# Optimization experiments

Hardware: AMD Instinct MI355X
Metric: run time of the kernel (lower is better)

The kernel has to match this reference:

```python
import jax, jax.numpy as jnp
import numpy as np

B, P, K = 32, 1000, 40          # events, hits per event, kNN neighbors
N = B * P                        # total nodes
IN_C, D, S = 64, 32, 3           # in_channels, d_shape, space_dimensions
EPS = 1e-5


def _bn(x, g, b):
    # BatchNorm1d in training mode: batch statistics over the node axis
    m = x.mean(0)
    v = x.var(0)
    return (x - m) * jax.lax.rsqrt(v + EPS) * g + b


def setup_inputs() -> dict:
    key = jax.random.key(0)
    ks = jax.random.split(key, 16)

    def xavier(k, shape):
        lim = float(np.sqrt(6.0 / (shape[0] + shape[1])))
        return jax.random.uniform(k, shape, minval=-lim, maxval=lim, dtype=jnp.float32)

    return {
        "x": jax.random.normal(ks[0], (N, IN_C), dtype=jnp.float32),
        "original_coords": jax.random.normal(ks[1], (N, S), dtype=jnp.float32),
        "batch": jnp.repeat(jnp.arange(B, dtype=jnp.int64), P),
        # pre-gravnet MLP
        "pre_w1": xavier(ks[2], (IN_C, D)), "pre_b1": jnp.zeros((D,), jnp.float32),
        "pre_w2": xavier(ks[3], (D, D)),   "pre_b2": jnp.zeros((D,), jnp.float32),
        "bn1_g": jnp.ones((D,), jnp.float32), "bn1_b": jnp.zeros((D,), jnp.float32),
        # GravNetConv linears
        "lin_s_w": xavier(ks[4], (D, S)),  "lin_s_b": jnp.zeros((S,), jnp.float32),
        "lin_h_w": xavier(ks[5], (D, D)),  "lin_h_b": jnp.zeros((D,), jnp.float32),
        "out1_w": xavier(ks[6], (D, D)),                      # no bias (PyG lin_out1)
        "out2_w": xavier(ks[7], (2 * D, D)), "out2_b": jnp.zeros((D,), jnp.float32),
        # post-gravnet MLP (input = out_channels + space + d_shape = 67)
        "post_w1": xavier(ks[8], (D + S + D, D)), "post_b1": jnp.zeros((D,), jnp.float32),
        "post_w2": xavier(ks[9], (D, D)),         "post_b2": jnp.zeros((D,), jnp.float32),
        "bn2_g": jnp.ones((D,), jnp.float32), "bn2_b": jnp.zeros((D,), jnp.float32),
    }


def reference(x, original_coords, batch,
              pre_w1, pre_b1, pre_w2, pre_b2, bn1_g, bn1_b,
              lin_s_w, lin_s_b, lin_h_w, lin_h_b,
              out1_w, out2_w, out2_b,
              post_w1, post_b1, post_w2, post_b2, bn2_g, bn2_b):
    # pre-MLP + BN
    h = jax.nn.elu(jax.nn.elu(x @ pre_w1 + pre_b1) @ pre_w2 + pre_b2)
    h = _bn(h, bn1_g, bn1_b)
    x_input = h

    # GravNetConv: learned space + feature projections
    s = h @ lin_s_w + lin_s_b            # [N, S] gncoords
    feat = h @ lin_h_w + lin_h_b         # [N, D]

    sb = s.reshape(B, P, S)
    fb = feat.reshape(B, P, D)
    # dynamic kNN within each event (includes self, as in torch_cluster knn)
    d2 = jnp.sum((sb[:, :, None, :] - sb[:, None, :, :]) ** 2, axis=-1)  # [B,P,P]
    neg_d2, idx = jax.lax.top_k(-d2, K)                                   # [B,P,K]
    w = jnp.exp(10.0 * neg_d2)           # exp(-10 * d^2) edge weights

    neigh = jax.vmap(lambda f, i: f[i])(fb, idx)  # [B,P,K,D] gather
    msg = neigh * w[..., None]
    aggr = jnp.concatenate([msg.mean(axis=2), msg.max(axis=2)], axis=-1)  # [B,P,2D]
    aggr = aggr.reshape(N, 2 * D)

    xgn = h @ out1_w + aggr @ out2_w + out2_b   # [N, D]

    # concat + post-MLP + BN
    cat = jnp.concatenate([xgn, s, x_input], axis=1)  # [N, D+S+D]
    out = jax.nn.elu(jax.nn.elu(cat @ post_w1 + post_b1) @ post_w2 + post_b2)
    out = _bn(out, bn2_g, bn2_b)
    return out
```

## Files before the change

### kernel.cpp

```cpp
#include <hip/hip_runtime.h>
#include <math.h>

#define NN 32000
#define PP 1000
#define KK 40
#define INC 64
#define DD 32
#define EPSV 1e-5

#define OB_H64 0UL
#define OB_S64 8192000UL
#define OB_F32 8960000UL
#define OB_A32 13056000UL
#define OB_P1  21248000UL
#define OB_P2  21504000UL
#define OB_S32 21760000UL
#define OB_ST1 22144000UL
#define OB_ST2 22144512UL

__device__ __forceinline__ double elud(double v){ return v > 0.0 ? v : expm1(v); }
__device__ __forceinline__ float eluf(float v){ return v > 0.f ? v : expm1f(v); }

__global__ __launch_bounds__(128) void k_pre(const float* __restrict__ x,
    const float* __restrict__ w1, const float* __restrict__ b1,
    const float* __restrict__ w2, const float* __restrict__ b2,
    char* __restrict__ ws)
{
  __shared__ double lw1[INC*DD];
  __shared__ double lw2[DD*DD];
  __shared__ double lb1[DD], lb2[DD];
  __shared__ double wpart[2][64];
  int tid = threadIdx.x;
  int nodeBase = blockIdx.x * 64;
  for (int i = tid; i < INC*DD; i += 128) lw1[i] = (double)w1[i];
  for (int i = tid; i < DD*DD; i += 128) lw2[i] = (double)w2[i];
  if (tid < DD){ lb1[tid] = (double)b1[tid]; lb2[tid] = (double)b2[tid]; }
  __syncthreads();

  int nl = tid >> 1, half = tid & 1;
  int node = nodeBase + nl;
  const float* xr = x + (size_t)node * INC;
  double acc[16];
#pragma unroll
  for (int c = 0; c < 16; ++c) acc[c] = lb1[half*16 + c];
#pragma unroll 4
  for (int k = 0; k < INC; ++k){
    double xv = (double)xr[k];
#pragma unroll
    for (int c = 0; c < 16; ++c) acc[c] = fma(xv, lw1[k*DD + half*16 + c], acc[c]);
  }
  double h1o[16];
#pragma unroll
  for (int c = 0; c < 16; ++c) h1o[c] = elud(acc[c]);
  double h1f[DD];
#pragma unroll
  for (int i = 0; i < 16; ++i){
    double p = __shfl_xor(h1o[i], 1);
    h1f[i]      = half ? p : h1o[i];
    h1f[16 + i] = half ? h1o[i] : p;
  }
#pragma unroll
  for (int c = 0; c < 16; ++c) acc[c] = lb2[half*16 + c];
#pragma unroll 4
  for (int k = 0; k < DD; ++k){
    double hk = h1f[k];
#pragma unroll
    for (int c = 0; c < 16; ++c) acc[c] = fma(hk, lw2[k*DD + half*16 + c], acc[c]);
  }
  double h2[16];
#pragma unroll
  for (int c = 0; c < 16; ++c) h2[c] = elud(acc[c]);
  double* hT = (double*)(ws + OB_H64);
#pragma unroll
  for (int c = 0; c < 16; ++c) hT[(size_t)(half*16 + c)*NN + node] = h2[c];

  double s[16], q[16];
#pragma unroll
  for (int i = 0; i < 16; ++i){ s[i] = h2[i]; q[i] = h2[i]*h2[i]; }
#pragma unroll
  for (int o = 2; o <= 32; o <<= 1){
#pragma unroll
    for (int i = 0; i < 16; ++i){ s[i] += __shfl_xor(s[i], o); q[i] += __shfl_xor(q[i], o); }
  }
  int lane = tid & 63, wid = tid >> 6;
  if (lane < 2){
#pragma unroll
    for (int i = 0; i < 16; ++i){
      wpart[wid][lane*16 + i]      = s[i];
      wpart[wid][32 + lane*16 + i] = q[i];
    }
  }
  __syncthreads();
  if (tid < 64)
    ((double*)(ws + OB_P1))[blockIdx.x*64 + tid] = wpart[0][tid] + wpart[1][tid];
}

__global__ __launch_bounds__(128) void k_stats(const double* __restrict__ part,
    double* __restrict__ stats, int nrows)
{
  __shared__ double ls[128], lq[128];
  int c = blockIdx.x;
  int t = threadIdx.x;
  double s = 0.0, q = 0.0;
  for (int r = t; r < nrows; r += 128){
    s += part[r*64 + c];
    q += part[r*64 + 32 + c];
  }
  ls[t] = s; lq[t] = q;
  __syncthreads();
  for (int o = 64; o > 0; o >>= 1){
    if (t < o){ ls[t] += ls[t+o]; lq[t] += lq[t+o]; }
    __syncthreads();
  }
  if (t == 0){
    double m = ls[0] / (double)NN;
    double qq = lq[0] / (double)NN;
    stats[c] = m;
    stats[32+c] = 1.0 / sqrt(qq - m*m + EPSV);
  }
}

__global__ __launch_bounds__(128) void k_sfeat(
    const float* __restrict__ sw, const float* __restrict__ sb,
    const float* __restrict__ hw, const float* __restrict__ hb,
    const float* __restrict__ g, const float* __restrict__ b,
    char* __restrict__ ws)
{
  __shared__ double lsw[DD*3], lsb[3], lstat[64], lgd[DD], lbd[DD];
  __shared__ float lhw[DD*DD], lhb[DD];
  int tid = threadIdx.x;
  for (int i = tid; i < DD*3; i += 128) lsw[i] = (double)sw[i];
  for (int i = tid; i < DD*DD; i += 128) lhw[i] = hw[i];
  if (tid < 3) lsb[tid] = (double)sb[tid];
  if (tid < DD){ lhb[tid] = hb[tid]; lgd[tid] = (double)g[tid]; lbd[tid] = (double)b[tid]; }
  if (tid >= 64 && tid < 128) lstat[tid-64] = ((const double*)(ws + OB_ST1))[tid-64];
  __syncthreads();
  int nl = tid >> 1, p = tid & 1;
  int node = blockIdx.x*64 + nl;
  const double* hT = (const double*)(ws + OB_H64);
  double ho[16];
#pragma unroll
  for (int i = 0; i < 16; ++i){
    int c = p*16 + i;
    double xv = hT[(size_t)c*NN + node];
    ho[i] = (xv - lstat[c]) * lstat[32+c] * lgd[c] + lbd[c];
  }
  double hf[DD];
#pragma unroll
  for (int i = 0; i < 16; ++i){
    double pr = __shfl_xor(ho[i], 1);
    hf[i]      = p ? pr : ho[i];
    hf[16 + i] = p ? ho[i] : pr;
  }
  double* sT = (double*)(ws + OB_S64);
  float* s32 = (float*)(ws + OB_S32) + (size_t)node*3;
  if (p == 0){
    double s0 = lsb[0], s2 = lsb[2];
#pragma unroll
    for (int k = 0; k < DD; ++k){
      s0 = fma(hf[k], lsw[k*3+0], s0);
      s2 = fma(hf[k], lsw[k*3+2], s2);
    }
    sT[node] = s0; sT[2*NN + node] = s2;
    s32[0] = (float)s0; s32[2] = (float)s2;
  } else {
    double s1 = lsb[1];
#pragma unroll
    for (int k = 0; k < DD; ++k) s1 = fma(hf[k], lsw[k*3+1], s1);
    sT[NN + node] = s1;
    s32[1] = (float)s1;
  }
  float hv[DD];
#pragma unroll
  for (int c = 0; c < DD; ++c) hv[c] = (float)hf[c];
  float f[16];
#pragma unroll
  for (int i = 0; i < 16; ++i) f[i] = lhb[p*16 + i];
#pragma unroll 4
  for (int k = 0; k < DD; ++k){
    float hk = hv[k];
#pragma unroll
    for (int i = 0; i < 16; ++i) f[i] = fmaf(hk, lhw[k*DD + p*16 + i], f[i]);
  }
  float* frow = (float*)(ws + OB_F32) + (size_t)node*DD + p*16;
#pragma unroll
  for (int u = 0; u < 4; ++u)
    ((float4*)frow)[u] = make_float4(f[4*u], f[4*u+1], f[4*u+2], f[4*u+3]);
}

__global__ __launch_bounds__(256) void k_knn(char* __restrict__ ws)
{
  __shared__ int   lds_cand[4][64];
  __shared__ int   lds_j[4][KK];
  __shared__ float lds_w[4][KK];
  const double* sT = (const double*)(ws + OB_S64);
  const float*  fp = (const float*)(ws + OB_F32);
  float* ap = (float*)(ws + OB_A32);
  int tid = threadIdx.x;
  int lane = tid & 63, wid = tid >> 6;
  int n = blockIdx.x * 4 + wid;
  int e = n / PP;
  int base = e * PP;
  const float* s32 = (const float*)(ws + OB_S32) + (size_t)base*3;
  int nl = n - base;
  float sxf = s32[nl*3+0], syf = s32[nl*3+1], szf = s32[nl*3+2];

  float d2f[16];
#pragma unroll
  for (int t = 0; t < 16; ++t){
    int j = lane + 64*t;
    float d2 = __builtin_inff();
    if (j < PP){
      const float* p = s32 + j*3;
      float dx = p[0] - sxf, dy = p[1] - syf, dz = p[2] - szf;
      d2 = (dx*dx + dy*dy) + dz*dz;
    }
    d2f[t] = d2;
  }
  float lmin = d2f[0];
#pragma unroll
  for (int t = 1; t < 16; ++t) lmin = fminf(lmin, d2f[t]);
  float glo = lmin, ghi = lmin;
#pragma unroll
  for (int o = 32; o > 0; o >>= 1){
    glo = fminf(glo, __shfl_xor(glo, o));
    ghi = fmaxf(ghi, __shfl_xor(ghi, o));
  }
  unsigned lo = __float_as_uint(glo), hi = __float_as_uint(ghi);
  while (lo < hi){
    unsigned mid = lo + ((hi - lo) >> 1);
    float midf = __uint_as_float(mid);
    int c = 0;
#pragma unroll
    for (int t = 0; t < 16; ++t) c += __popcll(__ballot(d2f[t] <= midf));
    if (c >= KK){
      if (c <= 56){ lo = mid; break; }
      hi = mid;
    } else lo = mid + 1;
  }
  float T = __uint_as_float(lo) * 1.0015f;

  unsigned long long lml = (1ull << lane) - 1ull;
  int cnt = 0;
#pragma unroll
  for (int t = 0; t < 16; ++t){
    bool sel = d2f[t] <= T;
    unsigned long long m = __ballot(sel);
    if (sel){
      int pos = cnt + __popcll(m & lml);
      if (pos < 64) lds_cand[wid][pos] = lane + 64*t;
    }
    cnt += __popcll(m);
  }
  if (cnt > 64) cnt = 64;

  double sx = sT[n], sy = sT[NN + n], sz = sT[2*NN + n];
  int jl = (lane < cnt) ? lds_cand[wid][lane] : -1;
  double d2l = __builtin_inf();
  if (jl >= 0){
    int jj = base + jl;
    double dx = sT[jj] - sx, dy = sT[NN + jj] - sy, dz = sT[2*NN + jj] - sz;
    d2l = (dx*dx + dy*dy) + dz*dz;
  }
  unsigned long long bits = (unsigned long long)__double_as_longlong(d2l);
  unsigned khi = (unsigned)(bits >> 32);
  unsigned klo = (unsigned)bits;
  unsigned blo = (jl >= 0) ? khi : 0xFFFFFFFFu;
  unsigned bhi = (jl >= 0) ? khi : 0u;
#pragma unroll
  for (int o = 32; o > 0; o >>= 1){
    blo = min(blo, (unsigned)__shfl_xor((int)blo, o));
    bhi = max(bhi, (unsigned)__shfl_xor((int)bhi, o));
  }
  unsigned l1 = blo, h1 = bhi;
  while (l1 < h1){
    unsigned mid = l1 + ((h1 - l1) >> 1);
    int c = __popcll(__ballot(khi <= mid));
    if (c >= KK) h1 = mid; else l1 = mid + 1;
  }
  unsigned H2 = l1;
  int cLT = __popcll(__ballot(khi < H2));
  int r = KK - cLT;
  unsigned l2 = 0u, h2 = 0xFFFFFFFFu;
  while (l2 < h2){
    unsigned mid = l2 + ((h2 - l2) >> 1);
    int c = __popcll(__ballot(khi == H2 && klo <= mid));
    if (c >= r) h2 = mid; else l2 = mid + 1;
  }
  unsigned L2v = l2;
  int cLT2 = __popcll(__ballot(khi == H2 && klo < L2v));
  int r2 = r - cLT2;
  bool dup = (khi == H2) && (klo == L2v);
  unsigned long long dupm = __ballot(dup);
  int rank = 0;
  if (dup){
    unsigned long long mm = dupm;
    while (mm){
      int l = __builtin_ctzll(mm);
      mm &= mm - 1;
      if (lds_cand[wid][l] < jl) rank++;
    }
  }
  bool sel40 = (khi < H2) || (khi == H2 && klo < L2v) || (dup && rank < r2);
  unsigned long long selm = __ballot(sel40);
  if (sel40){
    int pos = __popcll(selm & lml);
    lds_j[wid][pos] = jl;
    lds_w[wid][pos] = expf(-10.f * (float)d2l);
  }

  int half = lane >> 5, ch = lane & 31;
  float accm = 0.f, accx = -__builtin_inff();
#pragma unroll
  for (int c0 = 0; c0 < 2; ++c0){
    float fv[10], wv[10];
#pragma unroll
    for (int it = 0; it < 10; ++it){
      int si = 2*(c0*10 + it) + half;
      int j = lds_j[wid][si];
      wv[it] = lds_w[wid][si];
      fv[it] = fp[((base + j) << 5) + ch];
    }
#pragma unroll
    for (int it = 0; it < 10; ++it){
      float m = wv[it] * fv[it];
      accm += m;
      accx = fmaxf(accx, m);
    }
  }
  accm += __shfl_xor(accm, 32);
  accx = fmaxf(accx, __shfl_xor(accx, 32));
  if (lane < DD){
    ap[(size_t)n*64 + lane]      = accm * (1.f/KK);
    ap[(size_t)n*64 + DD + lane] = accx;
  }
}

__global__ __launch_bounds__(128) void k_post(
    const float* __restrict__ g, const float* __restrict__ b,
    const float* __restrict__ o1w, const float* __restrict__ o2w,
    const float* __restrict__ o2b,
    const float* __restrict__ p1w, const float* __restrict__ p1b,
    const float* __restrict__ p2w, const float* __restrict__ p2b,
    char* __restrict__ ws)
{
  __shared__ float l1[DD*DD], l2[2*DD*DD], lp1[67*DD], lp2[DD*DD];
  __shared__ float l2b[DD], lp1b[DD], lp2b[DD];
  __shared__ double lstat[64], lgd[DD], lbd[DD];
  __shared__ double wpart[2][64];
  int tid = threadIdx.x;
  for (int i = tid; i < DD*DD; i += 128) l1[i] = o1w[i];
  for (int i = tid; i < 2*DD*DD; i += 128) l2[i] = o2w[i];
  for (int i = tid; i < 67*DD; i += 128) lp1[i] = p1w[i];
  for (int i = tid; i < DD*DD; i += 128) lp2[i] = p2w[i];
  if (tid < DD){ l2b[tid] = o2b[tid]; lp1b[tid] = p1b[tid]; lp2b[tid] = p2b[tid];
                 lgd[tid] = (double)g[tid]; lbd[tid] = (double)b[tid]; }
  if (tid >= 64 && tid < 128) lstat[tid-64] = ((const double*)(ws + OB_ST1))[tid-64];
  __syncthreads();
  int node = blockIdx.x*128 + tid;
  const double* hT = (const double*)(ws + OB_H64);
  float hv[DD];
#pragma unroll 4
  for (int c = 0; c < DD; ++c){
    double xv = hT[(size_t)c*NN + node];
    hv[c] = (float)((xv - lstat[c]) * lstat[32+c] * lgd[c] + lbd[c]);
  }
  float xg[DD];
#pragma unroll
  for (int c = 0; c < DD; ++c) xg[c] = l2b[c];
#pragma unroll 4
  for (int k = 0; k < DD; ++k){
    float hk = hv[k];
#pragma unroll
    for (int c = 0; c < DD; ++c) xg[c] = fmaf(hk, l1[k*DD+c], xg[c]);
  }
  const float4* ar = (const float4*)((const float*)(ws + OB_A32) + (size_t)node*64);
#pragma unroll 2
  for (int k4 = 0; k4 < 16; ++k4){
    float4 a = ar[k4];
    float as[4] = {a.x, a.y, a.z, a.w};
#pragma unroll
    for (int u = 0; u < 4; ++u){
      int k = k4*4 + u;
#pragma unroll
      for (int c = 0; c < DD; ++c) xg[c] = fmaf(as[u], l2[k*DD+c], xg[c]);
    }
  }
  float t1[DD];
#pragma unroll
  for (int c = 0; c < DD; ++c) t1[c] = lp1b[c];
#pragma unroll 4
  for (int k = 0; k < DD; ++k){
    float v = xg[k];
#pragma unroll
    for (int c = 0; c < DD; ++c) t1[c] = fmaf(v, lp1[k*DD+c], t1[c]);
  }
  {
    const double* sT = (const double*)(ws + OB_S64);
    float s0 = (float)sT[node], s1 = (float)sT[NN+node], s2 = (float)sT[2*NN+node];
#pragma unroll
    for (int c = 0; c < DD; ++c){
      t1[c] = fmaf(s0, lp1[32*DD+c], t1[c]);
      t1[c] = fmaf(s1, lp1[33*DD+c], t1[c]);
      t1[c] = fmaf(s2, lp1[34*DD+c], t1[c]);
    }
  }
#pragma unroll 4
  for (int k = 0; k < DD; ++k){
    float v = hv[k];
#pragma unroll
    for (int c = 0; c < DD; ++c) t1[c] = fmaf(v, lp1[(35+k)*DD+c], t1[c]);
  }
#pragma unroll
  for (int c = 0; c < DD; ++c) t1[c] = eluf(t1[c]);
  float t2[DD];
#pragma unroll
  for (int c = 0; c < DD; ++c) t2[c] = lp2b[c];
#pragma unroll 4
  for (int k = 0; k < DD; ++k){
    float v = t1[k];
#pragma unroll
    for (int c = 0; c < DD; ++c) t2[c] = fmaf(v, lp2[k*DD+c], t2[c]);
  }
#pragma unroll
  for (int c = 0; c < DD; ++c) t2[c] = eluf(t2[c]);
  float* tr = (float*)(ws + OB_F32) + (size_t)node*DD;
#pragma unroll
  for (int u = 0; u < 8; ++u)
    ((float4*)tr)[u] = make_float4(t2[4*u], t2[4*u+1], t2[4*u+2], t2[4*u+3]);

  int lane = tid & 63, wid = tid >> 6;
#pragma unroll
  for (int hlf = 0; hlf < 2; ++hlf){
    double s[16], q[16];
#pragma unroll
    for (int i = 0; i < 16; ++i){ double xv = (double)t2[hlf*16 + i]; s[i] = xv; q[i] = xv*xv; }
#pragma unroll
    for (int o = 32; o > 0; o >>= 1){
#pragma unroll
      for (int i = 0; i < 16; ++i){ s[i] += __shfl_xor(s[i], o); q[i] += __shfl_xor(q[i], o); }
    }
    if (lane == 0){
#pragma unroll
      for (int i = 0; i < 16; ++i){
        wpart[wid][hlf*16 + i] = s[i];
        wpart[wid][32 + hlf*16 + i] = q[i];
      }
    }
  }
  __syncthreads();
  if (tid < 64)
    ((double*)(ws + OB_P2))[blockIdx.x*64 + tid] = wpart[0][tid] + wpart[1][tid];
}

__global__ __launch_bounds__(256) void k_bnout(
    const float* __restrict__ g, const float* __restrict__ b,
    const char* __restrict__ ws, float* __restrict__ out)
{
  __shared__ float lstat[64], lg[DD], lb[DD];
  int tid = threadIdx.x;
  if (tid < 64) lstat[tid] = (float)((const double*)(ws + OB_ST2))[tid];
  if (tid >= 64 && tid < 96){ lg[tid-64] = g[tid-64]; lb[tid-64] = b[tid-64]; }
  __syncthreads();
  int node = blockIdx.x*256 + tid;
  const float4* tr = (const float4*)((const float*)(ws + OB_F32) + (size_t)node*DD);
  float4* orow = (float4*)(out + (size_t)node*DD);
#pragma unroll
  for (int i = 0; i < 8; ++i){
    float4 v = tr[i];
    float vv[4] = {v.x, v.y, v.z, v.w};
#pragma unroll
    for (int u = 0; u < 4; ++u){
      int c = 4*i + u;
      vv[u] = (vv[u] - lstat[c]) * lstat[32+c] * lg[c] + lb[c];
    }
    orow[i] = make_float4(vv[0], vv[1], vv[2], vv[3]);
  }
}

extern "C" void kernel_launch(void* const* d_in, const int* in_sizes, int n_in,
                              void* d_out, int out_size, void* d_ws, size_t ws_size,
                              hipStream_t stream)
{
  const float* x       = (const float*)d_in[0];
  const float* pre_w1  = (const float*)d_in[3];
  const float* pre_b1  = (const float*)d_in[4];
  const float* pre_w2  = (const float*)d_in[5];
  const float* pre_b2  = (const float*)d_in[6];
  const float* bn1_g   = (const float*)d_in[7];
  const float* bn1_b   = (const float*)d_in[8];
  const float* lin_s_w = (const float*)d_in[9];
  const float* lin_s_b = (const float*)d_in[10];
  const float* lin_h_w = (const float*)d_in[11];
  const float* lin_h_b = (const float*)d_in[12];
  const float* out1_w  = (const float*)d_in[13];
  const float* out2_w  = (const float*)d_in[14];
  const float* out2_b  = (const float*)d_in[15];
  const float* post_w1 = (const float*)d_in[16];
  const float* post_b1 = (const float*)d_in[17];
  const float* post_w2 = (const float*)d_in[18];
  const float* post_b2 = (const float*)d_in[19];
  const float* bn2_g   = (const float*)d_in[20];
  const float* bn2_b   = (const float*)d_in[21];
  char* ws  = (char*)d_ws;
  float* out = (float*)d_out;

  k_pre  <<<500, 128, 0, stream>>>(x, pre_w1, pre_b1, pre_w2, pre_b2, ws);
  k_stats<<<32, 128, 0, stream>>>((const double*)(ws + OB_P1), (double*)(ws + OB_ST1), 500);
  k_sfeat<<<500, 128, 0, stream>>>(lin_s_w, lin_s_b, lin_h_w, lin_h_b, bn1_g, bn1_b, ws);
  k_knn  <<<8000, 256, 0, stream>>>(ws);
  k_post <<<250, 128, 0, stream>>>(bn1_g, bn1_b, out1_w, out2_w, out2_b,
                                   post_w1, post_b1, post_w2, post_b2, ws);
  k_stats<<<32, 128, 0, stream>>>((const double*)(ws + OB_P2), (double*)(ws + OB_ST2), 250);
  k_bnout<<<125, 256, 0, stream>>>(bn2_g, bn2_b, ws, out);
}
```

Before: 188.9 us.

## Split pre-MLP across four lanes per node; use expanded-norm kNN distance keys

```diff
diff --git a/kernel.cpp b/kernel.cpp
--- a/kernel.cpp
+++ b/kernel.cpp
@@ -13,10 +13,10 @@
 #define OB_F32 8960000UL
 #define OB_A32 13056000UL
 #define OB_P1  21248000UL
-#define OB_P2  21504000UL
-#define OB_S32 21760000UL
-#define OB_ST1 22144000UL
-#define OB_ST2 22144512UL
+#define OB_P2  21760000UL
+#define OB_S32 21888000UL
+#define OB_ST1 22400000UL
+#define OB_ST2 22400512UL
 
 __device__ __forceinline__ double elud(double v){ return v > 0.0 ? v : expm1(v); }
 __device__ __forceinline__ float eluf(float v){ return v > 0.f ? v : expm1f(v); }
@@ -31,63 +31,63 @@
   __shared__ double lb1[DD], lb2[DD];
   __shared__ double wpart[2][64];
   int tid = threadIdx.x;
-  int nodeBase = blockIdx.x * 64;
+  int nodeBase = blockIdx.x * 32;
   for (int i = tid; i < INC*DD; i += 128) lw1[i] = (double)w1[i];
   for (int i = tid; i < DD*DD; i += 128) lw2[i] = (double)w2[i];
   if (tid < DD){ lb1[tid] = (double)b1[tid]; lb2[tid] = (double)b2[tid]; }
   __syncthreads();
 
-  int nl = tid >> 1, half = tid & 1;
+  int nl = tid >> 2, q = tid & 3;
   int node = nodeBase + nl;
   const float* xr = x + (size_t)node * INC;
-  double acc[16];
-#pragma unroll
-  for (int c = 0; c < 16; ++c) acc[c] = lb1[half*16 + c];
-#pragma unroll 4
+  double acc[8];
+#pragma unroll
+  for (int c = 0; c < 8; ++c) acc[c] = lb1[q*8 + c];
+#pragma unroll 8
   for (int k = 0; k < INC; ++k){
     double xv = (double)xr[k];
 #pragma unroll
-    for (int c = 0; c < 16; ++c) acc[c] = fma(xv, lw1[k*DD + half*16 + c], acc[c]);
-  }
-  double h1o[16];
-#pragma unroll
-  for (int c = 0; c < 16; ++c) h1o[c] = elud(acc[c]);
+    for (int c = 0; c < 8; ++c) acc[c] = fma(xv, lw1[k*DD + q*8 + c], acc[c]);
+  }
+  double h1o[8];
+#pragma unroll
+  for (int c = 0; c < 8; ++c) h1o[c] = elud(acc[c]);
   double h1f[DD];
 #pragma unroll
-  for (int i = 0; i < 16; ++i){
-    double p = __shfl_xor(h1o[i], 1);
-    h1f[i]      = half ? p : h1o[i];
-    h1f[16 + i] = half ? h1o[i] : p;
-  }
-#pragma unroll
-  for (int c = 0; c < 16; ++c) acc[c] = lb2[half*16 + c];
-#pragma unroll 4
+  for (int b = 0; b < 4; ++b){
+#pragma unroll
+    for (int i = 0; i < 8; ++i)
+      h1f[b*8 + i] = __shfl_xor(h1o[i], q ^ b);
+  }
+#pragma unroll
+  for (int c = 0; c < 8; ++c) acc[c] = lb2[q*8 + c];
+#pragma unroll 8
   for (int k = 0; k < DD; ++k){
     double hk = h1f[k];
 #pragma unroll
-    for (int c = 0; c < 16; ++c) acc[c] = fma(hk, lw2[k*DD + half*16 + c], acc[c]);
-  }
-  double h2[16];
-#pragma unroll
-  for (int c = 0; c < 16; ++c) h2[c] = elud(acc[c]);
+    for (int c = 0; c < 8; ++c) acc[c] = fma(hk, lw2[k*DD + q*8 + c], acc[c]);
+  }
+  double h2[8];
+#pragma unroll
+  for (int c = 0; c < 8; ++c) h2[c] = elud(acc[c]);
   double* hT = (double*)(ws + OB_H64);
 #pragma unroll
-  for (int c = 0; c < 16; ++c) hT[(size_t)(half*16 + c)*NN + node] = h2[c];
-
-  double s[16], q[16];
-#pragma unroll
-  for (int i = 0; i < 16; ++i){ s[i] = h2[i]; q[i] = h2[i]*h2[i]; }
-#pragma unroll
-  for (int o = 2; o <= 32; o <<= 1){
-#pragma unroll
-    for (int i = 0; i < 16; ++i){ s[i] += __shfl_xor(s[i], o); q[i] += __shfl_xor(q[i], o); }
+  for (int c = 0; c < 8; ++c) hT[(size_t)(q*8 + c)*NN + node] = h2[c];
+
+  double s[8], qv[8];
+#pragma unroll
+  for (int i = 0; i < 8; ++i){ s[i] = h2[i]; qv[i] = h2[i]*h2[i]; }
+#pragma unroll
+  for (int o = 4; o <= 32; o <<= 1){
+#pragma unroll
+    for (int i = 0; i < 8; ++i){ s[i] += __shfl_xor(s[i], o); qv[i] += __shfl_xor(qv[i], o); }
   }
   int lane = tid & 63, wid = tid >> 6;
-  if (lane < 2){
-#pragma unroll
-    for (int i = 0; i < 16; ++i){
-      wpart[wid][lane*16 + i]      = s[i];
-      wpart[wid][32 + lane*16 + i] = q[i];
+  if (lane < 4){
+#pragma unroll
+    for (int i = 0; i < 8; ++i){
+      wpart[wid][lane*8 + i]      = s[i];
+      wpart[wid][32 + lane*8 + i] = qv[i];
     }
   }
   __syncthreads();
@@ -153,7 +153,7 @@
     hf[16 + i] = p ? ho[i] : pr;
   }
   double* sT = (double*)(ws + OB_S64);
-  float* s32 = (float*)(ws + OB_S32) + (size_t)node*3;
+  double v0 = 0.0, v1 = 0.0, v2 = 0.0;
   if (p == 0){
     double s0 = lsb[0], s2 = lsb[2];
 #pragma unroll
@@ -162,13 +162,22 @@
       s2 = fma(hf[k], lsw[k*3+2], s2);
     }
     sT[node] = s0; sT[2*NN + node] = s2;
-    s32[0] = (float)s0; s32[2] = (float)s2;
+    v0 = s0; v2 = s2;
   } else {
     double s1 = lsb[1];
 #pragma unroll
     for (int k = 0; k < DD; ++k) s1 = fma(hf[k], lsw[k*3+1], s1);
     sT[NN + node] = s1;
-    s32[1] = (float)s1;
+    v1 = s1;
+  }
+  {
+    float f0 = (float)v0, f1 = (float)v1, f2 = (float)v2;
+    float g0 = __shfl_xor(f0, 1);
+    float g2 = __shfl_xor(f2, 1);
+    if (p == 1){
+      float r = fmaf(g2, g2, fmaf(f1, f1, g0*g0));
+      ((float4*)(ws + OB_S32))[node] = make_float4(g0, f1, g2, r);
+    }
   }
   float hv[DD];
 #pragma unroll
@@ -201,21 +210,25 @@
   int n = blockIdx.x * 4 + wid;
   int e = n / PP;
   int base = e * PP;
-  const float* s32 = (const float*)(ws + OB_S32) + (size_t)base*3;
+  const float4* s4 = (const float4*)(ws + OB_S32) + base;
   int nl = n - base;
-  float sxf = s32[nl*3+0], syf = s32[nl*3+1], szf = s32[nl*3+2];
+  float4 qv = s4[nl];
+  float m2x = -2.f*qv.x, m2y = -2.f*qv.y, m2z = -2.f*qv.z;
+  float rq = qv.w;
 
   float d2f[16];
 #pragma unroll
   for (int t = 0; t < 16; ++t){
     int j = lane + 64*t;
-    float d2 = __builtin_inff();
+    float key = __builtin_inff();
     if (j < PP){
-      const float* p = s32 + j*3;
-      float dx = p[0] - sxf, dy = p[1] - syf, dz = p[2] - szf;
-      d2 = (dx*dx + dy*dy) + dz*dz;
-    }
-    d2f[t] = d2;
+      float4 p = s4[j];
+      float u = fmaf(p.x, m2x, p.w);
+      u = fmaf(p.y, m2y, u);
+      u = fmaf(p.z, m2z, u);
+      key = fmaxf(u + rq, 0.f);
+    }
+    d2f[t] = key;
   }
   float lmin = d2f[0];
 #pragma unroll
@@ -238,7 +251,7 @@
       hi = mid;
     } else lo = mid + 1;
   }
-  float T = __uint_as_float(lo) * 1.0015f;
+  float T = __uint_as_float(lo) * 1.0015f + 4e-6f;
 
   unsigned long long lml = (1ull << lane) - 1ull;
   int cnt = 0;
@@ -505,8 +518,8 @@
   char* ws  = (char*)d_ws;
   float* out = (float*)d_out;
 
-  k_pre  <<<500, 128, 0, stream>>>(x, pre_w1, pre_b1, pre_w2, pre_b2, ws);
-  k_stats<<<32, 128, 0, stream>>>((const double*)(ws + OB_P1), (double*)(ws + OB_ST1), 500);
+  k_pre  <<<1000, 128, 0, stream>>>(x, pre_w1, pre_b1, pre_w2, pre_b2, ws);
+  k_stats<<<32, 128, 0, stream>>>((const double*)(ws + OB_P1), (double*)(ws + OB_ST1), 1000);
   k_sfeat<<<500, 128, 0, stream>>>(lin_s_w, lin_s_b, lin_h_w, lin_h_b, bn1_g, bn1_b, ws);
   k_knn  <<<8000, 256, 0, stream>>>(ws);
   k_post <<<250, 128, 0, stream>>>(bn1_g, bn1_b, out1_w, out2_w, out2_b,
```

Result: faster. 181.6 us (-3.9%).
